# Kernel tuning notes

Hardware: AMD Instinct MI355X
Metric: run time of the kernel (lower is better)

The kernel has to match this reference:

```python
import jax, jax.numpy as jnp
import numpy as np

B, V, C, NQ, H, PTS, FFN = 2, 6, 128, 1200, 8, 4, 256
SHAPES = [(112, 200), (56, 100), (28, 50), (14, 25)]
LVLS = len(SHAPES)
LTOT = sum(h * w for h, w in SHAPES)
STARTS = np.cumsum([0] + [h * w for h, w in SHAPES])[:-1].tolist()


def _ln(x, g, b):
    m = jnp.mean(x, -1, keepdims=True)
    v = jnp.var(x, -1, keepdims=True)
    return (x - m) * jax.lax.rsqrt(v + 1e-5) * g + b


def _mlp(x, w1, b1, w2, b2):
    return jax.nn.relu(x @ w1 + b1) @ w2 + b2


def setup_inputs():
    ks = iter(jax.random.split(jax.random.key(0), 64))
    def rn(*shape):
        return jax.random.normal(next(ks), shape, jnp.float32) * 0.02
    inp = {}
    inp["img_query_feat"] = jax.random.normal(next(ks), (B, C, NQ), jnp.float32)
    inp["normal_img_query_pos"] = jax.random.normal(next(ks), (B, NQ, 2), jnp.float32)
    for i, (h, w) in enumerate(SHAPES):
        inp["img_feat%d" % i] = jax.random.normal(next(ks), (B, V, C, h, w), jnp.float32)
    inp["normal_img_feats_pos_stack"] = jax.random.uniform(next(ks), (1, LTOT, 2), jnp.float32)
    inp["sp_w1"] = rn(2, C); inp["sp_b1"] = rn(C); inp["sp_w2"] = rn(C, C); inp["sp_b2"] = rn(C)
    inp["cp_w1"] = rn(2, C); inp["cp_b1"] = rn(C); inp["cp_w2"] = rn(C, C); inp["cp_b2"] = rn(C)
    inp["sa_wqkv"] = rn(C, 3 * C); inp["sa_bqkv"] = rn(3 * C); inp["sa_wo"] = rn(C, C); inp["sa_bo"] = rn(C)
    inp["ln1_g"] = jnp.ones((C,), jnp.float32); inp["ln1_b"] = jnp.zeros((C,), jnp.float32)
    inp["d_val_w"] = rn(C, C); inp["d_val_b"] = rn(C)
    inp["d_off_w"] = rn(C, H * LVLS * PTS * 2); inp["d_off_b"] = rn(H * LVLS * PTS * 2)
    inp["d_attn_w"] = rn(C, H * LVLS * PTS); inp["d_attn_b"] = rn(H * LVLS * PTS)
    inp["d_out_w"] = rn(C, C); inp["d_out_b"] = rn(C)
    inp["ln2_g"] = jnp.ones((C,), jnp.float32); inp["ln2_b"] = jnp.zeros((C,), jnp.float32)
    inp["ffn_w1"] = rn(C, FFN); inp["ffn_b1"] = rn(FFN); inp["ffn_w2"] = rn(FFN, C); inp["ffn_b2"] = rn(C)
    inp["ln3_g"] = jnp.ones((C,), jnp.float32); inp["ln3_b"] = jnp.zeros((C,), jnp.float32)
    inp["ph_w1"] = rn(C, C); inp["ph_b1"] = rn(C); inp["ph_w2"] = rn(C, 6); inp["ph_b2"] = rn(6)
    inp["img_query_view"] = jax.random.randint(next(ks), (B, NQ), 0, V)
    return inp


def _forward(img_query_view, img_query_feat, normal_img_query_pos, img_feat0, img_feat1, img_feat2, img_feat3, normal_img_feats_pos_stack, sp_w1, sp_b1, sp_w2, sp_b2, cp_w1, cp_b1, cp_w2, cp_b2, sa_wqkv, sa_bqkv, sa_wo, sa_bo, ln1_g, ln1_b, d_val_w, d_val_b, d_off_w, d_off_b, d_attn_w, d_attn_b, d_out_w, d_out_b, ln2_g, ln2_b, ffn_w1, ffn_b1, ffn_w2, ffn_b2, ln3_g, ln3_b, ph_w1, ph_b1, ph_w2, ph_b2):
    # flatten multi-scale feats: [B, V, C, LTOT]
    feats = jnp.concatenate([f.reshape(B, V, C, -1) for f in (img_feat0, img_feat1, img_feat2, img_feat3)], axis=3)
    ref = jax.nn.sigmoid(normal_img_query_pos)  # [B,NQ,2], shared across levels
    qpe = _mlp(normal_img_query_pos, sp_w1, sp_b1, sp_w2, sp_b2)  # [B,NQ,C] self posembed
    kpe = _mlp(normal_img_feats_pos_stack[0], cp_w1, cp_b1, cp_w2, cp_b2)  # [LTOT,C] cross posembed
    # value projection of (key + key_pos_embed), per view
    value = jnp.einsum('bvcl,cd->bvld', feats, d_val_w) + kpe @ d_val_w + d_val_b  # [B,V,LTOT,C]
    value_flat = value.reshape(B, V * LTOT, C)
    x = img_query_feat.transpose(0, 2, 1)  # [B,NQ,C]
    # ragged per-view grouping: queries interact only within their own view
    same_view = img_query_view[:, :, None] == img_query_view[:, None, :]
    counts = jax.vmap(lambda v: jnp.bincount(v, length=V))(img_query_view)  # [B,V]
    valid = jnp.take_along_axis(counts, img_query_view, axis=1) > 1  # views with <=1 query are skipped
    Ch = C // H
    # --- self attention (masked to same view) ---
    qkv = (x + qpe) @ sa_wqkv + sa_bqkv
    q, k, v = jnp.split(qkv, 3, axis=-1)
    q = q.reshape(B, NQ, H, Ch); k = k.reshape(B, NQ, H, Ch); v = v.reshape(B, NQ, H, Ch)
    logits = jnp.einsum('bnhd,bmhd->bhnm', q, k) / float(np.sqrt(Ch))
    logits = jnp.where(same_view[:, None], logits, -1e9)
    attn = jax.nn.softmax(logits, axis=-1)
    sa_out = jnp.einsum('bhnm,bmhd->bnhd', attn, v).reshape(B, NQ, C) @ sa_wo + sa_bo
    x = _ln(x + sa_out, ln1_g, ln1_b)
    # --- multi-scale deformable cross attention, view-routed per query ---
    qc = x + qpe
    off = (qc @ d_off_w + d_off_b).reshape(B, NQ, H, LVLS, PTS, 2)
    aw = jax.nn.softmax((qc @ d_attn_w + d_attn_b).reshape(B, NQ, H, LVLS * PTS), axis=-1).reshape(B, NQ, H, LVLS, PTS)
    normalizer = jnp.array([[w, h] for h, w in SHAPES], jnp.float32)  # (w,h) per level
    loc = ref[:, :, None, None, None, :] + off / normalizer[None, None, None, :, None, :]
    base = (img_query_view * LTOT)[:, :, None, None].astype(jnp.int32)  # route query to its view
    eyeH = jnp.eye(H, dtype=x.dtype)
    out = jnp.zeros((B, NQ, H, Ch), x.dtype)
    for l, (h, w) in enumerate(SHAPES):
        lx = loc[:, :, :, l, :, 0] * w - 0.5  # grid_sample align_corners=False convention
        ly = loc[:, :, :, l, :, 1] * h - 0.5  # [B,NQ,H,PTS]
        x0 = jnp.floor(lx); y0 = jnp.floor(ly)
        fx = lx - x0; fy = ly - y0
        x0i = x0.astype(jnp.int32); y0i = y0.astype(jnp.int32)
        samp = jnp.zeros((B, NQ, H, PTS, Ch), x.dtype)
        for dy in (0, 1):
            for dx in (0, 1):
                xi = x0i + dx; yi = y0i + dy
                wgt = (fx if dx else 1.0 - fx) * (fy if dy else 1.0 - fy)
                ok = (xi >= 0) & (xi < w) & (yi >= 0) & (yi < h)  # zero padding
                idx = base + STARTS[l] + jnp.clip(yi, 0, h - 1) * w + jnp.clip(xi, 0, w - 1)
                g = jnp.take_along_axis(value_flat, idx.reshape(B, -1)[:, :, None], axis=1)
                g = g.reshape(B, NQ, H, PTS, H, Ch)
                g = jnp.einsum('bnhpqc,hq->bnhpc', g, eyeH)  # head h uses its own channel slice
                samp = samp + jnp.where(ok[..., None], wgt[..., None], 0.0) * g
        out = out + jnp.einsum('bnhp,bnhpc->bnhc', aw[:, :, :, l], samp)
    ca_out = out.reshape(B, NQ, C) @ d_out_w + d_out_b
    x = _ln(x + ca_out, ln2_g, ln2_b)
    x = _ln(x + _mlp(x, ffn_w1, ffn_b1, ffn_w2, ffn_b2), ln3_g, ln3_b)
    x = jnp.where(valid[..., None], x, 0.0)  # skipped views stay zero (scatter-back semantics)
    # --- prediction head: center_offset [B,6,NQ] ---
    res = _mlp(x, ph_w1, ph_b1, ph_w2, ph_b2).transpose(0, 2, 1)
    center_raw = res[:, :2] + normal_img_query_pos.transpose(0, 2, 1)
    new_pos = jax.lax.stop_gradient(center_raw).transpose(0, 2, 1)  # supervision2d=True update
    center = jax.nn.sigmoid(center_raw)
    offs = jax.nn.sigmoid(res[:, 2:])
    bw = offs[:, 0] + offs[:, 2]
    bh = offs[:, 1] + offs[:, 3]
    cx = (2.0 * center[:, 0] - offs[:, 0] + offs[:, 2]) * 0.5
    cy = (2.0 * center[:, 1] - offs[:, 1] + offs[:, 3]) * 0.5
    bbox = jax.lax.stop_gradient(jnp.stack([cx, cy, bw, bh], axis=1))
    return (x.transpose(0, 2, 1), new_pos, center, offs, bbox)


def reference(img_query_feat, normal_img_query_pos, img_feat0, img_feat1, img_feat2, img_feat3, normal_img_feats_pos_stack, sp_w1, sp_b1, sp_w2, sp_b2, cp_w1, cp_b1, cp_w2, cp_b2, sa_wqkv, sa_bqkv, sa_wo, sa_bo, ln1_g, ln1_b, d_val_w, d_val_b, d_off_w, d_off_b, d_attn_w, d_attn_b, d_out_w, d_out_b, ln2_g, ln2_b, ffn_w1, ffn_b1, ffn_w2, ffn_b2, ln3_g, ln3_b, ph_w1, ph_b1, ph_w2, ph_b2, img_query_view):
    return _forward(img_query_view, img_query_feat, normal_img_query_pos, img_feat0, img_feat1, img_feat2, img_feat3, normal_img_feats_pos_stack, sp_w1, sp_b1, sp_w2, sp_b2, cp_w1, cp_b1, cp_w2, cp_b2, sa_wqkv, sa_bqkv, sa_wo, sa_bo, ln1_g, ln1_b, d_val_w, d_val_b, d_off_w, d_off_b, d_attn_w, d_attn_b, d_out_w, d_out_b, ln2_g, ln2_b, ffn_w1, ffn_b1, ffn_w2, ffn_b2, ln3_g, ln3_b, ph_w1, ph_b1, ph_w2, ph_b2)
```

## Files before the change

kernel.cpp:

```cpp
#include <hip/hip_runtime.h>
#include <hip/hip_bf16.h>
#include <math.h>

#define DEV __device__ __forceinline__

#define BB 2
#define VV 6
#define CC 128
#define NQ 1200
#define HH 8
#define PTSN 4
#define FFND 256
#define LVLSN 4
#define LTOT 29750
#define NROWS (BB*NQ)

__constant__ int c_W[4] = {200,100,50,25};
__constant__ int c_H[4] = {112,56,28,14};
__constant__ int c_S[4] = {0,22400,28000,29400};

DEV float bflo(unsigned u){ union{unsigned i; float f;}x; x.i = u<<16; return x.f; }
DEV float bfhi(unsigned u){ union{unsigned i; float f;}x; x.i = u&0xffff0000u; return x.f; }
DEV unsigned short f2bf(float f){ union{float f; unsigned i;}x; x.f=f; unsigned i=x.i;
  return (unsigned short)((i + 0x7fffu + ((i>>16)&1u))>>16); }
DEV unsigned addbf2(unsigned a, unsigned b){
  float lo = bflo(a)+bflo(b); float hi = bfhi(a)+bfhi(b);
  return (unsigned)f2bf(lo) | ((unsigned)f2bf(hi)<<16);
}
DEV float sigm(float z){ return 1.f/(1.f+__expf(-z)); }

typedef __attribute__((ext_vector_type(8))) short bf16x8;
typedef __attribute__((ext_vector_type(4))) float f32x4;

__global__ void k_misc(const int* __restrict__ view, int* __restrict__ order,
                       int* __restrict__ counts,
                       const float* __restrict__ vw, unsigned short* __restrict__ wt,
                       const float* __restrict__ cw2, unsigned short* __restrict__ cw2t,
                       const float* __restrict__ iqf, float* __restrict__ x,
                       const float* __restrict__ pos,
                       const float* __restrict__ w1, const float* __restrict__ b1,
                       const float* __restrict__ w2, const float* __restrict__ b2,
                       float* __restrict__ qpe){
  int bid = blockIdx.x;
  int t = threadIdx.x;
  if(bid < BB){
    if(t < 64){
      int b = bid; int lane = t;
      int base0=0,base1=0,base2=0,base3=0,base4=0,base5=0;
      for(int c0=0;c0<NQ;c0+=64){
        int n = c0 + lane;
        int v = (n<NQ) ? view[b*NQ+n] : -1;
        unsigned long long lower = (lane==63)? 0x7fffffffffffffffull : ((1ull<<lane)-1ull);
        #define BUCKET_STEP(VVV, BASE) { \
          unsigned long long mk = __ballot(v==VVV); \
          if(v==VVV){ int r = BASE + __popcll(mk & lower); order[(b*VV+VVV)*NQ + r] = n; } \
          BASE += __popcll(mk); }
        BUCKET_STEP(0, base0) BUCKET_STEP(1, base1) BUCKET_STEP(2, base2)
        BUCKET_STEP(3, base3) BUCKET_STEP(4, base4) BUCKET_STEP(5, base5)
        #undef BUCKET_STEP
      }
      if(lane==0){
        counts[b*VV+0]=base0; counts[b*VV+1]=base1; counts[b*VV+2]=base2;
        counts[b*VV+3]=base3; counts[b*VV+4]=base4; counts[b*VV+5]=base5;
      }
    }
  } else if(bid < BB+16){
    int d0 = (bid-BB)*8;
    __shared__ float s[128][9];
    #pragma unroll
    for(int p=0;p<4;p++){ int i = t + p*256; int c = i>>3, dd = i&7;
      s[c][dd] = vw[c*128 + d0 + dd]; }
    __syncthreads();
    #pragma unroll
    for(int p=0;p<4;p++){ int i = t + p*256; int dd = i>>7, c = i&127;
      wt[(size_t)(d0+dd)*128 + c] = f2bf(s[c][dd]); }
  } else if(bid < BB+32){
    int d0 = (bid-BB-16)*8;
    __shared__ float s[128][9];
    #pragma unroll
    for(int p=0;p<4;p++){ int i = t + p*256; int c = i>>3, dd = i&7;
      s[c][dd] = cw2[c*128 + d0 + dd]; }
    __syncthreads();
    #pragma unroll
    for(int p=0;p<4;p++){ int i = t + p*256; int dd = i>>7, c = i&127;
      cw2t[(size_t)(d0+dd)*128 + c] = f2bf(s[c][dd]); }
  } else if(bid < BB+32+76){
    __shared__ float tile[128][33];
    int idx = bid - (BB+32);
    int b = idx/38; int n0 = (idx%38)*32;
    for(int i=t;i<128*32;i+=256){ int c=i>>5, nn=i&31; int n=n0+nn;
      tile[c][nn] = (n<NQ)? iqf[((size_t)b*CC + c)*NQ + n] : 0.f; }
    __syncthreads();
    for(int i=t;i<32*128;i+=256){ int nn=i>>7, c=i&127;
      int n=n0+nn; if(n<NQ) x[((size_t)b*NQ+n)*128 + c] = tile[c][nn]; }
  } else {
    __shared__ float hid[4][128];
    int row0 = (bid - (BB+32+76))*4;
    int r = t>>7, d = t&127;
    #pragma unroll
    for(int rr=r; rr<4; rr+=2){
      int row = row0 + rr;
      float p0 = pos[row*2+0], p1 = pos[row*2+1];
      hid[rr][d] = fmaxf(p0*w1[d] + p1*w1[128+d] + b1[d], 0.f);
    }
    __syncthreads();
    #pragma unroll
    for(int rr=r; rr<4; rr+=2){
      float acc = b2[d];
      #pragma unroll 4
      for(int c=0;c<128;c++) acc += hid[rr][c]*w2[c*128 + d];
      qpe[(size_t)(row0+rr)*128+d] = acc;
    }
  }
}

__global__ void __launch_bounds__(256) k_kvpe2(
    const float* __restrict__ kpos,
    const float* __restrict__ cw1, const float* __restrict__ cb1,
    const unsigned short* __restrict__ cw2t, const float* __restrict__ cb2,
    const unsigned short* __restrict__ wt, const float* __restrict__ vb,
    unsigned short* __restrict__ kvpe){
  __shared__ unsigned short h_t[64][136];
  __shared__ unsigned short k_t[64][136];
  int t = threadIdx.x;
  int r0 = blockIdx.x*64;
  int lane = t&63, wave = t>>6;
  int fr = lane&15, kg = lane>>4;

  int p = t & 63;
  int d0 = p*2;
  float w1a0 = cw1[d0],     w1a1 = cw1[d0+1];
  float w1b0 = cw1[128+d0], w1b1 = cw1[128+d0+1];
  float b10 = cb1[d0], b11 = cb1[d0+1];
  #pragma unroll 4
  for(int k=0;k<16;k++){
    int r = wave + k*4;
    int row = r0 + r;
    float p0=0.f, p1=0.f;
    if(row < LTOT){ p0 = kpos[row*2]; p1 = kpos[row*2+1]; }
    float h0 = fmaxf(p0*w1a0 + p1*w1b0 + b10, 0.f);
    float h1 = fmaxf(p0*w1a1 + p1*w1b1 + b11, 0.f);
    *reinterpret_cast<unsigned*>(&h_t[r][d0]) = (unsigned)f2bf(h0) | ((unsigned)f2bf(h1)<<16);
  }
  __syncthreads();

  f32x4 acc[4][2];
  #pragma unroll
  for(int i=0;i<4;i++)
    #pragma unroll
    for(int j=0;j<2;j++) acc[i][j] = (f32x4)0.f;
  #pragma unroll
  for(int ck=0; ck<4; ck++){
    int c0 = ck*32;
    bf16x8 bfr[2], af[4];
    #pragma unroll
    for(int j=0;j<2;j++){ int d = wave*32 + j*16 + fr;
      bfr[j] = *reinterpret_cast<const bf16x8*>(cw2t + (size_t)d*128 + c0 + kg*8); }
    #pragma unroll
    for(int i=0;i<4;i++) af[i] = *reinterpret_cast<const bf16x8*>(&h_t[i*16 + fr][c0 + kg*8]);
    #pragma unroll
    for(int i=0;i<4;i++)
      #pragma unroll
      for(int j=0;j<2;j++)
        acc[i][j] = __builtin_amdgcn_mfma_f32_16x16x32_bf16(af[i], bfr[j], acc[i][j], 0, 0, 0);
  }
  #pragma unroll
  for(int i=0;i<4;i++){
    int rbase = i*16 + kg*4;
    #pragma unroll
    for(int j=0;j<2;j++){
      int d = wave*32 + j*16 + fr;
      float bv_ = cb2[d];
      #pragma unroll
      for(int r=0;r<4;r++) k_t[rbase + r][d] = f2bf(acc[i][j][r] + bv_);
    }
  }
  __syncthreads();

  #pragma unroll
  for(int i=0;i<4;i++)
    #pragma unroll
    for(int j=0;j<2;j++) acc[i][j] = (f32x4)0.f;
  #pragma unroll
  for(int ck=0; ck<4; ck++){
    int c0 = ck*32;
    bf16x8 bfr[2], af[4];
    #pragma unroll
    for(int j=0;j<2;j++){ int d = wave*32 + j*16 + fr;
      bfr[j] = *reinterpret_cast<const bf16x8*>(wt + (size_t)d*128 + c0 + kg*8); }
    #pragma unroll
    for(int i=0;i<4;i++) af[i] = *reinterpret_cast<const bf16x8*>(&k_t[i*16 + fr][c0 + kg*8]);
    #pragma unroll
    for(int i=0;i<4;i++)
      #pragma unroll
      for(int j=0;j<2;j++)
        acc[i][j] = __builtin_amdgcn_mfma_f32_16x16x32_bf16(af[i], bfr[j], acc[i][j], 0, 0, 0);
  }
  __syncthreads();
  unsigned short (*c_l)[136] = h_t;
  #pragma unroll
  for(int i=0;i<4;i++){
    int rbase = i*16 + kg*4;
    #pragma unroll
    for(int j=0;j<2;j++){
      int d = wave*32 + j*16 + fr;
      float bv_ = vb[d];
      #pragma unroll
      for(int r=0;r<4;r++) c_l[rbase + r][d] = f2bf(acc[i][j][r] + bv_);
    }
  }
  __syncthreads();
  #pragma unroll
  for(int p4=0;p4<4;p4++){
    int i = t + p4*256;
    int row = i>>4, seg = i&15;
    int glr = r0 + row;
    if(glr < LTOT){
      uint4 cu = *reinterpret_cast<const uint4*>(&c_l[row][seg*8]);
      *reinterpret_cast<uint4*>(kvpe + (size_t)glr*CC + seg*8) = cu;
    }
  }
}

#define QKVB 300
__global__ void __launch_bounds__(256) k_value_qkv(
    const float* __restrict__ f0, const float* __restrict__ f1,
    const float* __restrict__ f2, const float* __restrict__ f3,
    const unsigned short* __restrict__ kvpe, const unsigned short* __restrict__ wt,
    unsigned short* __restrict__ value,
    const float* __restrict__ x, const float* __restrict__ qpe,
    const float* __restrict__ sa_wqkv, const float* __restrict__ sa_bqkv,
    float* __restrict__ qkv){
  __shared__ unsigned short a_t[64][136];
  __shared__ float s_q[8][128];
  int t = threadIdx.x;
  int bid = blockIdx.x;
  if(bid < QKVB){
    int r0 = bid*8;
    for(int i=t;i<1024;i+=256){ int r=i>>7, c=i&127;
      size_t row = (size_t)(r0+r);
      s_q[r][c] = x[row*128+c] + qpe[row*128+c]; }
    __syncthreads();
    for(int d=t; d<384; d+=256){
      float acc[8];
      #pragma unroll
      for(int r=0;r<8;r++) acc[r]=sa_bqkv[d];
      #pragma unroll 4
      for(int c=0;c<128;c++){ float wv = sa_wqkv[c*384+d];
        #pragma unroll
        for(int r=0;r<8;r++) acc[r] += s_q[r][c]*wv; }
      #pragma unroll
      for(int r=0;r<8;r++) qkv[(size_t)(r0+r)*384+d]=acc[r];
    }
    return;
  }
  int bxy = bid - QKVB;
  int bv = bxy % 12;
  int bx = bxy / 12;
  int lvl, tile;
  if(bx < 350){ lvl=0; tile=bx; }
  else if(bx < 438){ lvl=1; tile=bx-350; }
  else if(bx < 460){ lvl=2; tile=bx-438; }
  else { lvl=3; tile=bx-460; }
  const int HW = (lvl==0)?22400:(lvl==1)?5600:(lvl==2)?1400:350;
  const int startL = (lvl==0)?0:(lvl==1)?22400:(lvl==2)?28000:29400;
  const float* feat = (lvl==0)?f0:(lvl==1)?f1:(lvl==2)?f2:f3;
  const float* fbase = feat + (size_t)bv*128*(size_t)HW;
  int l0 = tile*64;

  int lane = t&63, wave = t>>6;
  int fr = lane&15, kg = lane>>4;

  int l_u = t & 63, oct0 = t>>6;
  int gl = l0 + l_u; bool ok = (gl < HW);
  const float* fcol = fbase + (size_t)(oct0*8)*HW + (ok ? gl : 0);

  float v32[4][8];
  #pragma unroll
  for(int q=0;q<4;q++)
    #pragma unroll
    for(int j=0;j<8;j++)
      v32[q][j] = ok ? fcol[(size_t)(q*32+j)*HW] : 0.f;

  #pragma unroll
  for(int q=0;q<4;q++){
    uint4 u;
    u.x = (unsigned)f2bf(v32[q][0]) | ((unsigned)f2bf(v32[q][1])<<16);
    u.y = (unsigned)f2bf(v32[q][2]) | ((unsigned)f2bf(v32[q][3])<<16);
    u.z = (unsigned)f2bf(v32[q][4]) | ((unsigned)f2bf(v32[q][5])<<16);
    u.w = (unsigned)f2bf(v32[q][6]) | ((unsigned)f2bf(v32[q][7])<<16);
    *reinterpret_cast<uint4*>(&a_t[l_u][oct0*8 + q*32]) = u;
  }
  __syncthreads();

  f32x4 acc[4][2];
  #pragma unroll
  for(int i=0;i<4;i++)
    #pragma unroll
    for(int j=0;j<2;j++) acc[i][j] = (f32x4)0.f;

  #pragma unroll
  for(int ck=0; ck<4; ck++){
    int c0 = ck*32;
    bf16x8 bfr[2];
    #pragma unroll
    for(int j=0;j<2;j++){
      int d = wave*32 + j*16 + fr;
      bfr[j] = *reinterpret_cast<const bf16x8*>(wt + (size_t)d*128 + c0 + kg*8);
    }
    bf16x8 af[4];
    #pragma unroll
    for(int i=0;i<4;i++) af[i] = *reinterpret_cast<const bf16x8*>(&a_t[i*16 + fr][c0 + kg*8]);
    #pragma unroll
    for(int i=0;i<4;i++)
      #pragma unroll
      for(int j=0;j<2;j++)
        acc[i][j] = __builtin_amdgcn_mfma_f32_16x16x32_bf16(af[i], bfr[j], acc[i][j], 0, 0, 0);
  }

  __syncthreads();
  unsigned short (*c_l)[136] = a_t;
  #pragma unroll
  for(int i=0;i<4;i++){
    int rbase = i*16 + kg*4;
    #pragma unroll
    for(int j=0;j<2;j++){
      int d = wave*32 + j*16 + fr;
      #pragma unroll
      for(int r=0;r<4;r++) c_l[rbase + r][d] = f2bf(acc[i][j][r]);
    }
  }
  __syncthreads();
  #pragma unroll
  for(int p=0;p<4;p++){
    int i = t + p*256;
    int row = i>>4, seg = i&15;
    int glr = l0 + row;
    if(glr < HW){
      uint4 cu = *reinterpret_cast<const uint4*>(&c_l[row][seg*8]);
      const uint4 ku = *reinterpret_cast<const uint4*>(kvpe + (size_t)(startL+glr)*CC + seg*8);
      uint4 ou;
      ou.x = addbf2(cu.x, ku.x); ou.y = addbf2(cu.y, ku.y);
      ou.z = addbf2(cu.z, ku.z); ou.w = addbf2(cu.w, ku.w);
      *reinterpret_cast<uint4*>(value + ((size_t)bv*LTOT + startL + glr)*CC + seg*8) = ou;
    }
  }
}

#define QT2 64
#define KT2 128
__global__ void __launch_bounds__(256) k_attn_v(const float* __restrict__ qkv,
        const int* __restrict__ order, const int* __restrict__ counts,
        float* __restrict__ att){
  int qt = blockIdx.x;
  int vh = blockIdx.y; int v = vh>>3, h = vh&7;
  int b = blockIdx.z;
  int C = counts[b*VV+v];
  int q0 = qt*QT2;
  if(q0 >= C) return;
  const int* ord = order + (size_t)(b*VV+v)*NQ;
  int t = threadIdx.x;
  __shared__ float q_s[QT2][17];
  __shared__ int qn_s[QT2];
  __shared__ float k_s[KT2][16];
  __shared__ float v_s[KT2][16];
  __shared__ float red[4][QT2][18];
  for(int i=t;i<QT2;i+=256){ int qi=q0+i; qn_s[i] = (qi<C)? ord[qi] : -1; }
  __syncthreads();
  for(int i=t;i<QT2*16;i+=256){ int r=i>>4,c=i&15; int n=qn_s[r];
    q_s[r][c] = (n>=0)? qkv[((size_t)b*NQ+n)*384 + h*16 + c] : 0.f; }
  int qi = t&63, sub = t>>6;
  float m = -1e30f, s = 0.f, acc[16];
  #pragma unroll
  for(int c=0;c<16;c++) acc[c]=0.f;
  for(int k0=0; k0<C; k0+=KT2){
    int kn = C-k0; if(kn>KT2) kn=KT2;
    __syncthreads();
    for(int i=t;i<KT2*16;i+=256){ int r=i>>4,c=i&15;
      float kv=0.f, vv=0.f;
      if(r<kn){ int n=ord[k0+r]; size_t base=((size_t)b*NQ+n)*384 + h*16 + c;
        kv = qkv[base+128]; vv = qkv[base+256]; }
      k_s[r][c]=kv; v_s[r][c]=vv; }
    __syncthreads();
    for(int mm=sub; mm<kn; mm+=4){
      float l=0.f;
      #pragma unroll
      for(int c=0;c<16;c++) l += q_s[qi][c]*k_s[mm][c];
      l *= 0.25f;
      float newm = fmaxf(m,l);
      float e = __expf(l - newm);
      if(newm > m){
        float rr = __expf(m - newm);
        s *= rr;
        #pragma unroll
        for(int c=0;c<16;c++) acc[c]*=rr;
        m = newm;
      }
      s += e;
      #pragma unroll
      for(int c=0;c<16;c++) acc[c] += e*v_s[mm][c];
    }
  }
  red[sub][qi][0]=m; red[sub][qi][1]=s;
  #pragma unroll
  for(int c=0;c<16;c++) red[sub][qi][2+c]=acc[c];
  __syncthreads();
  if(sub==0){
    int n = qn_s[qi];
    if(n>=0){
      float M=-1e30f;
      #pragma unroll
      for(int j=0;j<4;j++) M=fmaxf(M,red[j][qi][0]);
      float S=0.f; float o[16];
      #pragma unroll
      for(int c=0;c<16;c++) o[c]=0.f;
      #pragma unroll
      for(int j=0;j<4;j++){ float e=__expf(red[j][qi][0]-M); S += e*red[j][qi][1];
        #pragma unroll
        for(int c=0;c<16;c++) o[c] += e*red[j][qi][2+c]; }
      float inv = 1.f/S;
      #pragma unroll
      for(int c=0;c<16;c++) att[((size_t)b*NQ+n)*128 + h*16 + c] = o[c]*inv;
    }
  }
}

__global__ void __launch_bounds__(384) k_q2(
    const float* __restrict__ att, const float* __restrict__ sa_wo, const float* __restrict__ sa_bo,
    float* __restrict__ x, const float* __restrict__ ln1_g, const float* __restrict__ ln1_b,
    const float* __restrict__ qpe,
    const float* __restrict__ dow, const float* __restrict__ dob,
    const float* __restrict__ daw, const float* __restrict__ dab,
    float* __restrict__ offb, float* __restrict__ awb){
  int r0 = blockIdx.x*8; int t = threadIdx.x;
  __shared__ float s_att[8][128];
  __shared__ float s_qc[8][128];
  __shared__ float s_m[8][2][2];
  __shared__ float s_aw[8][130];
  for(int i=t;i<1024;i+=384){ int r=i>>7, c=i&127; s_att[r][c]=att[(size_t)(r0+r)*128+c]; }
  __syncthreads();
  int lane = t&63, wid = (t>>6)&1;
  float v[8];
  if(t < 128){
    int d = t;
    float acc[8];
    #pragma unroll
    for(int r=0;r<8;r++) acc[r]=sa_bo[d];
    #pragma unroll 4
    for(int c=0;c<128;c++){ float wv = sa_wo[c*128+d];
      #pragma unroll
      for(int r=0;r<8;r++) acc[r] += s_att[r][c]*wv; }
    #pragma unroll
    for(int r=0;r<8;r++){
      v[r] = acc[r] + x[(size_t)(r0+r)*128 + d];
      float s1=v[r], s2=v[r]*v[r];
      for(int o=32;o>0;o>>=1){ s1 += __shfl_down(s1,o); s2 += __shfl_down(s2,o); }
      if(lane==0){ s_m[r][wid][0]=s1; s_m[r][wid][1]=s2; }
    }
  }
  __syncthreads();
  if(t < 128){
    int d = t;
    #pragma unroll
    for(int r=0;r<8;r++){
      float S1=s_m[r][0][0]+s_m[r][1][0], S2=s_m[r][0][1]+s_m[r][1][1];
      float mean=S1*(1.f/128.f), var=S2*(1.f/128.f)-mean*mean;
      float rs=rsqrtf(var+1e-5f);
      float o=(v[r]-mean)*rs*ln1_g[d]+ln1_b[d];
      x[(size_t)(r0+r)*128+d]=o;
      s_qc[r][d]=o+qpe[(size_t)(r0+r)*128+d];
    }
  }
  __syncthreads();
  if(t < 256){
    int d = t;
    float acc[8];
    #pragma unroll
    for(int r=0;r<8;r++) acc[r]=dob[d];
    #pragma unroll 4
    for(int c=0;c<128;c++){ float wv = dow[(size_t)c*256+d];
      #pragma unroll
      for(int r=0;r<8;r++) acc[r] += s_qc[r][c]*wv; }
    #pragma unroll
    for(int r=0;r<8;r++) offb[(size_t)(r0+r)*256+d]=acc[r];
  } else {
    int d = t - 256;
    float acc[8];
    #pragma unroll
    for(int r=0;r<8;r++) acc[r]=dab[d];
    #pragma unroll 4
    for(int c=0;c<128;c++){ float wv = daw[(size_t)c*128+d];
      #pragma unroll
      for(int r=0;r<8;r++) acc[r] += s_qc[r][c]*wv; }
    #pragma unroll
    for(int r=0;r<8;r++) s_aw[r][d]=acc[r];
  }
  __syncthreads();
  if(t < 64){
    int r = t>>3, h = t&7;
    float mx=-1e30f;
    #pragma unroll
    for(int i=0;i<16;i++) mx = fmaxf(mx, s_aw[r][h*16+i]);
    float e[16]; float sm=0.f;
    #pragma unroll
    for(int i=0;i<16;i++){ e[i]=__expf(s_aw[r][h*16+i]-mx); sm+=e[i]; }
    float inv = 1.f/sm;
    #pragma unroll
    for(int i=0;i<16;i++) awb[(size_t)(r0+r)*128 + h*16+i] = e[i]*inv;
  }
}

__global__ void __launch_bounds__(128) k_tail2(
    const float* __restrict__ qpos, const int* __restrict__ view,
    const float* __restrict__ offb, const float* __restrict__ awb,
    const unsigned short* __restrict__ value,
    const float* __restrict__ dOw, const float* __restrict__ dOb,
    const float* __restrict__ xres,
    const float* __restrict__ ln2_g, const float* __restrict__ ln2_b,
    const float* __restrict__ fw1, const float* __restrict__ fb1,
    const float* __restrict__ fw2, const float* __restrict__ fb2,
    const float* __restrict__ ln3_g, const float* __restrict__ ln3_b,
    const float* __restrict__ pw1, const float* __restrict__ pb1,
    const float* __restrict__ pw2, const float* __restrict__ pb2,
    const int* __restrict__ counts, float* __restrict__ dout){
  int r0 = blockIdx.x*4; int d = threadIdx.x;
  __shared__ float s_a[4][256];
  __shared__ float s_x[4][128];
  __shared__ float s_m[4][2][2];
  __shared__ float s_res[4][6];
  __shared__ float sred[128][17];
  __shared__ float s_ca[4][128];
  int lane = d&63, wid = d>>6;

  int h = d>>4, lp = d&15, lvl = lp>>2;
  int w = c_W[lvl], hh = c_H[lvl];
  float samp[4][16]; float aw4[4];
  int vw4[4];
  #pragma unroll
  for(int r=0;r<4;r++){
    size_t row = (size_t)(r0+r);
    int b = (r0+r)/NQ;
    float rx = sigm(qpos[row*2]), ry = sigm(qpos[row*2+1]);
    int vw = view[row]; vw4[r]=vw;
    float ox = offb[row*256 + d*2], oy = offb[row*256 + d*2+1];
    aw4[r] = awb[row*128 + d];
    float lx = rx*(float)w + ox - 0.5f;
    float ly = ry*(float)hh + oy - 0.5f;
    float x0f = floorf(lx), y0f = floorf(ly);
    float fx = lx - x0f, fy = ly - y0f;
    int x0 = (int)x0f, y0 = (int)y0f;
    #pragma unroll
    for(int c=0;c<16;c++) samp[r][c]=0.f;
    size_t brow = ((size_t)(b*VV + vw))*LTOT + c_S[lvl];
    #pragma unroll
    for(int dy=0;dy<2;dy++){
      #pragma unroll
      for(int dx=0;dx<2;dx++){
        int xi=x0+dx, yi=y0+dy;
        if(xi<0||xi>=w||yi<0||yi>=hh) continue;
        float wt = (dx?fx:(1.f-fx))*(dy?fy:(1.f-fy));
        const uint4* vp = reinterpret_cast<const uint4*>(value + (brow + (size_t)yi*w + xi)*CC + h*16);
        uint4 u0 = vp[0], u1 = vp[1];
        samp[r][0] += wt*bflo(u0.x); samp[r][1] += wt*bfhi(u0.x);
        samp[r][2] += wt*bflo(u0.y); samp[r][3] += wt*bfhi(u0.y);
        samp[r][4] += wt*bflo(u0.z); samp[r][5] += wt*bfhi(u0.z);
        samp[r][6] += wt*bflo(u0.w); samp[r][7] += wt*bfhi(u0.w);
        samp[r][8] += wt*bflo(u1.x); samp[r][9] += wt*bfhi(u1.x);
        samp[r][10]+= wt*bflo(u1.y); samp[r][11]+= wt*bfhi(u1.y);
        samp[r][12]+= wt*bflo(u1.z); samp[r][13]+= wt*bfhi(u1.z);
        samp[r][14]+= wt*bflo(u1.w); samp[r][15]+= wt*bfhi(u1.w);
      }
    }
  }
  #pragma unroll
  for(int r=0;r<4;r++){
    #pragma unroll
    for(int c=0;c<16;c++) sred[d][c] = aw4[r]*samp[r][c];
    __syncthreads();
    int h2=d>>4, c2=d&15;
    float sum=0.f;
    #pragma unroll
    for(int j=0;j<16;j++) sum += sred[h2*16+j][c2];
    s_ca[r][d] = sum;
    __syncthreads();
  }

  #pragma unroll
  for(int r=0;r<4;r++) s_a[r][d] = s_ca[r][d];
  __syncthreads();
  float acc[4];
  #pragma unroll
  for(int r=0;r<4;r++) acc[r]=dOb[d];
  #pragma unroll 4
  for(int c=0;c<128;c++){ float wv = dOw[c*128+d];
    #pragma unroll
    for(int r=0;r<4;r++) acc[r] += s_a[r][c]*wv; }
  float v[4];
  #pragma unroll
  for(int r=0;r<4;r++){
    v[r] = acc[r] + xres[(size_t)(r0+r)*128 + d];
    float s1=v[r], s2=v[r]*v[r];
    for(int o=32;o>0;o>>=1){ s1 += __shfl_down(s1,o); s2 += __shfl_down(s2,o); }
    if(lane==0){ s_m[r][wid][0]=s1; s_m[r][wid][1]=s2; }
  }
  __syncthreads();
  #pragma unroll
  for(int r=0;r<4;r++){
    float S1=s_m[r][0][0]+s_m[r][1][0], S2=s_m[r][0][1]+s_m[r][1][1];
    float mean=S1*(1.f/128.f), var=S2*(1.f/128.f)-mean*mean;
    float rs=rsqrtf(var+1e-5f);
    s_x[r][d]=(v[r]-mean)*rs*ln2_g[d]+ln2_b[d];
  }
  __syncthreads();

  float a2a[4], a2b[4];
  #pragma unroll
  for(int r=0;r<4;r++){ a2a[r]=fb1[d]; a2b[r]=fb1[d+128]; }
  #pragma unroll 4
  for(int c=0;c<128;c++){ float w0 = fw1[c*256+d], w1_ = fw1[c*256+d+128];
    #pragma unroll
    for(int r=0;r<4;r++){ float xv = s_x[r][c]; a2a[r] += xv*w0; a2b[r] += xv*w1_; } }
  __syncthreads();
  #pragma unroll
  for(int r=0;r<4;r++){ s_a[r][d]=fmaxf(a2a[r],0.f); s_a[r][d+128]=fmaxf(a2b[r],0.f); }
  __syncthreads();

  float a3[4];
  #pragma unroll
  for(int r=0;r<4;r++) a3[r]=fb2[d];
  #pragma unroll 4
  for(int c=0;c<256;c++){ float wv = fw2[c*128+d];
    #pragma unroll
    for(int r=0;r<4;r++) a3[r] += s_a[r][c]*wv; }
  #pragma unroll
  for(int r=0;r<4;r++){
    v[r] = a3[r] + s_x[r][d];
    float s1=v[r], s2=v[r]*v[r];
    for(int o=32;o>0;o>>=1){ s1 += __shfl_down(s1,o); s2 += __shfl_down(s2,o); }
    if(lane==0){ s_m[r][wid][0]=s1; s_m[r][wid][1]=s2; }
  }
  __syncthreads();
  #pragma unroll
  for(int r=0;r<4;r++){
    float S1=s_m[r][0][0]+s_m[r][1][0], S2=s_m[r][0][1]+s_m[r][1][1];
    float mean=S1*(1.f/128.f), var=S2*(1.f/128.f)-mean*mean;
    float rs=rsqrtf(var+1e-5f);
    float o=(v[r]-mean)*rs*ln3_g[d]+ln3_b[d];
    int row=r0+r; int b=row/NQ, n=row%NQ;
    bool val = counts[b*VV + vw4[r]] > 1;
    float oz = val ? o : 0.f;
    s_x[r][d]=oz;
    dout[((size_t)b*CC + d)*NQ + n]=oz;
  }
  __syncthreads();

  float a4[4];
  #pragma unroll
  for(int r=0;r<4;r++) a4[r]=pb1[d];
  #pragma unroll 4
  for(int c=0;c<128;c++){ float wv = pw1[c*128+d];
    #pragma unroll
    for(int r=0;r<4;r++) a4[r] += s_x[r][c]*wv; }
  #pragma unroll
  for(int r=0;r<4;r++) s_a[r][d]=fmaxf(a4[r],0.f);
  __syncthreads();

  if(d < 24){
    int r = d/6, o = d%6;
    float a5 = pb2[o];
    #pragma unroll 4
    for(int c=0;c<128;c++) a5 += s_a[r][c]*pw2[c*6+o];
    s_res[r][o] = a5;
  }
  __syncthreads();
  if(d < 4){
    int r = d; int row = r0+r; int b=row/NQ, n=row%NQ;
    const int O1 = BB*CC*NQ;
    const int O2 = O1 + BB*NQ*2;
    const int O3 = O2 + BB*2*NQ;
    const int O4 = O3 + BB*4*NQ;
    float p0=qpos[row*2], p1=qpos[row*2+1];
    float cr0 = s_res[r][0]+p0, cr1 = s_res[r][1]+p1;
    dout[O1 + row*2]   = cr0;
    dout[O1 + row*2+1] = cr1;
    float cen0 = sigm(cr0), cen1 = sigm(cr1);
    dout[O2 + (b*2+0)*NQ + n] = cen0;
    dout[O2 + (b*2+1)*NQ + n] = cen1;
    float f0=sigm(s_res[r][2]), f1=sigm(s_res[r][3]), f2=sigm(s_res[r][4]), f3=sigm(s_res[r][5]);
    dout[O3 + (b*4+0)*NQ + n] = f0;
    dout[O3 + (b*4+1)*NQ + n] = f1;
    dout[O3 + (b*4+2)*NQ + n] = f2;
    dout[O3 + (b*4+3)*NQ + n] = f3;
    float bw=f0+f2, bh=f1+f3;
    float cx=(2.f*cen0 - f0 + f2)*0.5f;
    float cy=(2.f*cen1 - f1 + f3)*0.5f;
    dout[O4 + (b*4+0)*NQ + n] = cx;
    dout[O4 + (b*4+1)*NQ + n] = cy;
    dout[O4 + (b*4+2)*NQ + n] = bw;
    dout[O4 + (b*4+3)*NQ + n] = bh;
  }
}

extern "C" void kernel_launch(void* const* d_in, const int* in_sizes, int n_in,
                              void* d_out, int out_size, void* d_ws, size_t ws_size,
                              hipStream_t stream){
  (void)in_sizes; (void)n_in; (void)out_size; (void)ws_size;
  const float* in_iqf  = (const float*)d_in[0];
  const float* in_qpos = (const float*)d_in[1];
  const float* in_feat[4] = {(const float*)d_in[2],(const float*)d_in[3],(const float*)d_in[4],(const float*)d_in[5]};
  const float* in_kpos = (const float*)d_in[6];
  const float* sp_w1=(const float*)d_in[7], *sp_b1=(const float*)d_in[8], *sp_w2=(const float*)d_in[9], *sp_b2=(const float*)d_in[10];
  const float* cp_w1=(const float*)d_in[11], *cp_b1=(const float*)d_in[12], *cp_w2=(const float*)d_in[13], *cp_b2=(const float*)d_in[14];
  const float* sa_wqkv=(const float*)d_in[15], *sa_bqkv=(const float*)d_in[16], *sa_wo=(const float*)d_in[17], *sa_bo=(const float*)d_in[18];
  const float* ln1_g=(const float*)d_in[19], *ln1_b=(const float*)d_in[20];
  const float* dvw=(const float*)d_in[21], *dvb=(const float*)d_in[22];
  const float* dow=(const float*)d_in[23], *dob=(const float*)d_in[24];
  const float* daw=(const float*)d_in[25], *dab=(const float*)d_in[26];
  const float* dOw=(const float*)d_in[27], *dOb=(const float*)d_in[28];
  const float* ln2_g=(const float*)d_in[29], *ln2_b=(const float*)d_in[30];
  const float* fw1=(const float*)d_in[31], *fb1=(const float*)d_in[32], *fw2=(const float*)d_in[33], *fb2=(const float*)d_in[34];
  const float* ln3_g=(const float*)d_in[35], *ln3_b=(const float*)d_in[36];
  const float* pw1=(const float*)d_in[37], *pb1=(const float*)d_in[38], *pw2=(const float*)d_in[39], *pb2=(const float*)d_in[40];
  const int* in_view = (const int*)d_in[41];
  float* out = (float*)d_out;

  char* ws = (char*)d_ws;
  unsigned short* value = (unsigned short*)ws;
  unsigned short* kvpe  = (unsigned short*)(ws + 91392000);
  float* f = (float*)(ws + 91392000 + 7616000);
  float* qpe  = f;
  float* x    = f + 307200;
  float* qkv  = f + 614400;
  float* att  = f + 1536000;
  float* offb = f + 2150400;
  float* awb  = f + 2764800;
  int* counts = (int*)(f + 4300800);
  int* order  = (int*)(f + 4300816);
  unsigned short* wtb   = (unsigned short*)(f + 4315216);
  unsigned short* cw2tb = (unsigned short*)(f + 4323408);

  k_misc<<<dim3(BB+32+76+600),dim3(256),0,stream>>>(in_view,order,counts,dvw,wtb,
      cp_w2,cw2tb,in_iqf,x,in_qpos,sp_w1,sp_b1,sp_w2,sp_b2,qpe);
  k_kvpe2<<<dim3((LTOT+63)/64),dim3(256),0,stream>>>(in_kpos,cp_w1,cp_b1,cw2tb,cp_b2,wtb,dvb,kvpe);
  k_value_qkv<<<dim3(QKVB + 466*12),dim3(256),0,stream>>>(in_feat[0],in_feat[1],in_feat[2],in_feat[3],
      kvpe,wtb,value,x,qpe,sa_wqkv,sa_bqkv,qkv);
  k_attn_v<<<dim3((NQ+QT2-1)/QT2, VV*HH, BB),dim3(256),0,stream>>>(qkv,order,counts,att);
  k_q2<<<dim3(NROWS/8),dim3(384),0,stream>>>(att,sa_wo,sa_bo,x,ln1_g,ln1_b,qpe,
      dow,dob,daw,dab,offb,awb);
  k_tail2<<<dim3(NROWS/4),dim3(128),0,stream>>>(in_qpos,in_view,offb,awb,value,
      dOw,dOb,x,ln2_g,ln2_b,fw1,fb1,fw2,fb2,ln3_g,ln3_b,pw1,pb1,pw2,pb2,counts,out);
}
```

Before: 229.0 us.

## Regroup kernels so QKV runs with kvpe and attention overlaps value projection

Moves the self-attention QKV projection blocks into the kvpe kernel and folds the per-view self-attention into the value-projection kernel as extra blocks, with shared memory unioned between roles. One kernel launch goes away, and the small attention work can run alongside the bandwidth-heavy value projection instead of after it. The attention key tile shrinks from 128 to 64 to fit the shared-memory union, which means more tile iterations and more syncs per block. Attention blocks whose view has few queries exit early and leave idle slots in the grid.

```diff
diff --git a/kernel.cpp b/kernel.cpp
--- a/kernel.cpp
+++ b/kernel.cpp
@@ -114,16 +114,41 @@
   }
 }
 
-__global__ void __launch_bounds__(256) k_kvpe2(
+#define NKVPE 465
+__global__ void __launch_bounds__(256) k_kvpe_qkv(
     const float* __restrict__ kpos,
     const float* __restrict__ cw1, const float* __restrict__ cb1,
     const unsigned short* __restrict__ cw2t, const float* __restrict__ cb2,
     const unsigned short* __restrict__ wt, const float* __restrict__ vb,
-    unsigned short* __restrict__ kvpe){
+    unsigned short* __restrict__ kvpe,
+    const float* __restrict__ x, const float* __restrict__ qpe,
+    const float* __restrict__ sa_wqkv, const float* __restrict__ sa_bqkv,
+    float* __restrict__ qkv){
   __shared__ unsigned short h_t[64][136];
   __shared__ unsigned short k_t[64][136];
   int t = threadIdx.x;
-  int r0 = blockIdx.x*64;
+  int bid = blockIdx.x;
+  if(bid >= NKVPE){
+    float (*s_q)[128] = (float(*)[128])h_t;
+    int r0 = (bid - NKVPE)*8;
+    for(int i=t;i<1024;i+=256){ int r=i>>7, c=i&127;
+      size_t row = (size_t)(r0+r);
+      s_q[r][c] = x[row*128+c] + qpe[row*128+c]; }
+    __syncthreads();
+    for(int d=t; d<384; d+=256){
+      float acc[8];
+      #pragma unroll
+      for(int r=0;r<8;r++) acc[r]=sa_bqkv[d];
+      #pragma unroll 4
+      for(int c=0;c<128;c++){ float wv = sa_wqkv[c*384+d];
+        #pragma unroll
+        for(int r=0;r<8;r++) acc[r] += s_q[r][c]*wv; }
+      #pragma unroll
+      for(int r=0;r<8;r++) qkv[(size_t)(r0+r)*384+d]=acc[r];
+    }
+    return;
+  }
+  int r0 = bid*64;
   int lane = t&63, wave = t>>6;
   int fr = lane&15, kg = lane>>4;
 
@@ -222,39 +247,97 @@
   }
 }
 
-#define QKVB 300
-__global__ void __launch_bounds__(256) k_value_qkv(
+#define NATT (19*48*2)
+#define QT2 64
+#define KTA 64
+__global__ void __launch_bounds__(256) k_value_attn2(
     const float* __restrict__ f0, const float* __restrict__ f1,
     const float* __restrict__ f2, const float* __restrict__ f3,
     const unsigned short* __restrict__ kvpe, const unsigned short* __restrict__ wt,
     unsigned short* __restrict__ value,
-    const float* __restrict__ x, const float* __restrict__ qpe,
-    const float* __restrict__ sa_wqkv, const float* __restrict__ sa_bqkv,
-    float* __restrict__ qkv){
-  __shared__ unsigned short a_t[64][136];
-  __shared__ float s_q[8][128];
+    const float* __restrict__ qkv,
+    const int* __restrict__ order, const int* __restrict__ counts,
+    float* __restrict__ att){
+  __shared__ __align__(16) char smem[18688];
   int t = threadIdx.x;
   int bid = blockIdx.x;
-  if(bid < QKVB){
-    int r0 = bid*8;
-    for(int i=t;i<1024;i+=256){ int r=i>>7, c=i&127;
-      size_t row = (size_t)(r0+r);
-      s_q[r][c] = x[row*128+c] + qpe[row*128+c]; }
-    __syncthreads();
-    for(int d=t; d<384; d+=256){
-      float acc[8];
-      #pragma unroll
-      for(int r=0;r<8;r++) acc[r]=sa_bqkv[d];
-      #pragma unroll 4
-      for(int c=0;c<128;c++){ float wv = sa_wqkv[c*384+d];
+  if(bid < NATT){
+    int qt = bid % 19;
+    int vh = (bid/19) % 48;
+    int b  = bid/(19*48);
+    int v = vh>>3, h = vh&7;
+    int C = counts[b*VV+v];
+    int q0 = qt*QT2;
+    if(q0 >= C) return;
+    const int* ord = order + (size_t)(b*VV+v)*NQ;
+    float (*q_s)[17] = (float(*)[17])smem;
+    float (*k_s)[16] = (float(*)[16])(smem + 4352);
+    float (*v_s)[16] = (float(*)[16])(smem + 8448);
+    float (*red)[QT2][18] = (float(*)[QT2][18])smem;
+    int* qn_s = (int*)(smem + 18432);
+    for(int i=t;i<QT2;i+=256){ int qi=q0+i; qn_s[i] = (qi<C)? ord[qi] : -1; }
+    __syncthreads();
+    for(int i=t;i<QT2*16;i+=256){ int r=i>>4,c=i&15; int n=qn_s[r];
+      q_s[r][c] = (n>=0)? qkv[((size_t)b*NQ+n)*384 + h*16 + c] : 0.f; }
+    int qi = t&63, sub = t>>6;
+    float m = -1e30f, s = 0.f, acc[16];
+    #pragma unroll
+    for(int c=0;c<16;c++) acc[c]=0.f;
+    for(int k0=0; k0<C; k0+=KTA){
+      int kn = C-k0; if(kn>KTA) kn=KTA;
+      __syncthreads();
+      for(int i=t;i<KTA*16;i+=256){ int r=i>>4,c=i&15;
+        float kv=0.f, vv=0.f;
+        if(r<kn){ int n=ord[k0+r]; size_t base=((size_t)b*NQ+n)*384 + h*16 + c;
+          kv = qkv[base+128]; vv = qkv[base+256]; }
+        k_s[r][c]=kv; v_s[r][c]=vv; }
+      __syncthreads();
+      for(int mm=sub; mm<kn; mm+=4){
+        float l=0.f;
         #pragma unroll
-        for(int r=0;r<8;r++) acc[r] += s_q[r][c]*wv; }
-      #pragma unroll
-      for(int r=0;r<8;r++) qkv[(size_t)(r0+r)*384+d]=acc[r];
+        for(int c=0;c<16;c++) l += q_s[qi][c]*k_s[mm][c];
+        l *= 0.25f;
+        float newm = fmaxf(m,l);
+        float e = __expf(l - newm);
+        if(newm > m){
+          float rr = __expf(m - newm);
+          s *= rr;
+          #pragma unroll
+          for(int c=0;c<16;c++) acc[c]*=rr;
+          m = newm;
+        }
+        s += e;
+        #pragma unroll
+        for(int c=0;c<16;c++) acc[c] += e*v_s[mm][c];
+      }
+    }
+    __syncthreads();
+    red[sub][qi][0]=m; red[sub][qi][1]=s;
+    #pragma unroll
+    for(int c=0;c<16;c++) red[sub][qi][2+c]=acc[c];
+    __syncthreads();
+    if(sub==0){
+      int n = qn_s[qi];
+      if(n>=0){
+        float M=-1e30f;
+        #pragma unroll
+        for(int j=0;j<4;j++) M=fmaxf(M,red[j][qi][0]);
+        float S=0.f; float o[16];
+        #pragma unroll
+        for(int c=0;c<16;c++) o[c]=0.f;
+        #pragma unroll
+        for(int j=0;j<4;j++){ float e=__expf(red[j][qi][0]-M); S += e*red[j][qi][1];
+          #pragma unroll
+          for(int c=0;c<16;c++) o[c] += e*red[j][qi][2+c]; }
+        float inv = 1.f/S;
+        #pragma unroll
+        for(int c=0;c<16;c++) att[((size_t)b*NQ+n)*128 + h*16 + c] = o[c]*inv;
+      }
     }
     return;
   }
-  int bxy = bid - QKVB;
+  unsigned short (*a_t)[136] = (unsigned short(*)[136])smem;
+  int bxy = bid - NATT;
   int bv = bxy % 12;
   int bx = bxy / 12;
   int lvl, tile;
@@ -343,84 +426,6 @@
       ou.x = addbf2(cu.x, ku.x); ou.y = addbf2(cu.y, ku.y);
       ou.z = addbf2(cu.z, ku.z); ou.w = addbf2(cu.w, ku.w);
       *reinterpret_cast<uint4*>(value + ((size_t)bv*LTOT + startL + glr)*CC + seg*8) = ou;
-    }
-  }
-}
-
-#define QT2 64
-#define KT2 128
-__global__ void __launch_bounds__(256) k_attn_v(const float* __restrict__ qkv,
-        const int* __restrict__ order, const int* __restrict__ counts,
-        float* __restrict__ att){
-  int qt = blockIdx.x;
-  int vh = blockIdx.y; int v = vh>>3, h = vh&7;
-  int b = blockIdx.z;
-  int C = counts[b*VV+v];
-  int q0 = qt*QT2;
-  if(q0 >= C) return;
-  const int* ord = order + (size_t)(b*VV+v)*NQ;
-  int t = threadIdx.x;
-  __shared__ float q_s[QT2][17];
-  __shared__ int qn_s[QT2];
-  __shared__ float k_s[KT2][16];
-  __shared__ float v_s[KT2][16];
-  __shared__ float red[4][QT2][18];
-  for(int i=t;i<QT2;i+=256){ int qi=q0+i; qn_s[i] = (qi<C)? ord[qi] : -1; }
-  __syncthreads();
-  for(int i=t;i<QT2*16;i+=256){ int r=i>>4,c=i&15; int n=qn_s[r];
-    q_s[r][c] = (n>=0)? qkv[((size_t)b*NQ+n)*384 + h*16 + c] : 0.f; }
-  int qi = t&63, sub = t>>6;
-  float m = -1e30f, s = 0.f, acc[16];
-  #pragma unroll
-  for(int c=0;c<16;c++) acc[c]=0.f;
-  for(int k0=0; k0<C; k0+=KT2){
-    int kn = C-k0; if(kn>KT2) kn=KT2;
-    __syncthreads();
-    for(int i=t;i<KT2*16;i+=256){ int r=i>>4,c=i&15;
-      float kv=0.f, vv=0.f;
-      if(r<kn){ int n=ord[k0+r]; size_t base=((size_t)b*NQ+n)*384 + h*16 + c;
-        kv = qkv[base+128]; vv = qkv[base+256]; }
-      k_s[r][c]=kv; v_s[r][c]=vv; }
-    __syncthreads();
-    for(int mm=sub; mm<kn; mm+=4){
-      float l=0.f;
-      #pragma unroll
-      for(int c=0;c<16;c++) l += q_s[qi][c]*k_s[mm][c];
-      l *= 0.25f;
-      float newm = fmaxf(m,l);
-      float e = __expf(l - newm);
-      if(newm > m){
-        float rr = __expf(m - newm);
-        s *= rr;
-        #pragma unroll
-        for(int c=0;c<16;c++) acc[c]*=rr;
-        m = newm;
-      }
-      s += e;
-      #pragma unroll
-      for(int c=0;c<16;c++) acc[c] += e*v_s[mm][c];
-    }
-  }
-  red[sub][qi][0]=m; red[sub][qi][1]=s;
-  #pragma unroll
-  for(int c=0;c<16;c++) red[sub][qi][2+c]=acc[c];
-  __syncthreads();
-  if(sub==0){
-    int n = qn_s[qi];
-    if(n>=0){
-      float M=-1e30f;
-      #pragma unroll
-      for(int j=0;j<4;j++) M=fmaxf(M,red[j][qi][0]);
-      float S=0.f; float o[16];
-      #pragma unroll
-      for(int c=0;c<16;c++) o[c]=0.f;
-      #pragma unroll
-      for(int j=0;j<4;j++){ float e=__expf(red[j][qi][0]-M); S += e*red[j][qi][1];
-        #pragma unroll
-        for(int c=0;c<16;c++) o[c] += e*red[j][qi][2+c]; }
-      float inv = 1.f/S;
-      #pragma unroll
-      for(int c=0;c<16;c++) att[((size_t)b*NQ+n)*128 + h*16 + c] = o[c]*inv;
     }
   }
 }
@@ -741,10 +746,10 @@
 
   k_misc<<<dim3(BB+32+76+600),dim3(256),0,stream>>>(in_view,order,counts,dvw,wtb,
       cp_w2,cw2tb,in_iqf,x,in_qpos,sp_w1,sp_b1,sp_w2,sp_b2,qpe);
-  k_kvpe2<<<dim3((LTOT+63)/64),dim3(256),0,stream>>>(in_kpos,cp_w1,cp_b1,cw2tb,cp_b2,wtb,dvb,kvpe);
-  k_value_qkv<<<dim3(QKVB + 466*12),dim3(256),0,stream>>>(in_feat[0],in_feat[1],in_feat[2],in_feat[3],
-      kvpe,wtb,value,x,qpe,sa_wqkv,sa_bqkv,qkv);
-  k_attn_v<<<dim3((NQ+QT2-1)/QT2, VV*HH, BB),dim3(256),0,stream>>>(qkv,order,counts,att);
+  k_kvpe_qkv<<<dim3(NKVPE + 300),dim3(256),0,stream>>>(in_kpos,cp_w1,cp_b1,cw2tb,cp_b2,wtb,dvb,kvpe,
+      x,qpe,sa_wqkv,sa_bqkv,qkv);
+  k_value_attn2<<<dim3(NATT + 466*12),dim3(256),0,stream>>>(in_feat[0],in_feat[1],in_feat[2],in_feat[3],
+      kvpe,wtb,value,qkv,order,counts,att);
   k_q2<<<dim3(NROWS/8),dim3(384),0,stream>>>(att,sa_wo,sa_bo,x,ln1_g,ln1_b,qpe,
       dow,dob,daw,dab,offb,awb);
   k_tail2<<<dim3(NROWS/4),dim3(128),0,stream>>>(in_qpos,in_view,offb,awb,value,
```

Measured after the change: 212.1 us. 1.08x faster.
